# Kernel tuning notes

Measured on AMD Instinct MI355X. Metric: run time of the kernel, lower is better.

## Reference

```python
import jax, jax.numpy as jnp
import numpy as np

B = 16384      # batch of (user, item) interactions
N = 819200     # total packed implicit-history items (~50 per user)
U = 100000     # num_users
I = 100000     # num_items
D = 64         # emb_dim


def setup_inputs() -> dict:
    key = jax.random.key(0)
    ks = jax.random.split(key, 8)
    user_ids = jax.random.randint(ks[0], (B,), 0, U)
    item_ids = jax.random.randint(ks[1], (B,), 0, I)
    offsets = jnp.sort(jax.random.randint(ks[2], (B,), 0, N)).at[0].set(0)
    flat_implicit = jax.random.randint(ks[3], (N,), 0, I)
    user_emb = 0.1 * jax.random.normal(ks[4], (U, D), dtype=jnp.float32)
    item_emb = 0.1 * jax.random.normal(ks[5], (I, D), dtype=jnp.float32)
    implicit_item_emb = 0.1 * jax.random.normal(ks[6], (I, D), dtype=jnp.float32)
    user_bias = jnp.zeros((U, 1), dtype=jnp.float32)
    item_bias = jnp.zeros((I, 1), dtype=jnp.float32)
    global_bias = jnp.zeros((1,), dtype=jnp.float32)
    return {"user_ids": user_ids, "item_ids": item_ids, "offsets": offsets,
            "flat_implicit": flat_implicit, "user_emb": user_emb,
            "item_emb": item_emb, "implicit_item_emb": implicit_item_emb,
            "user_bias": user_bias, "item_bias": item_bias,
            "global_bias": global_bias}


def reference(user_ids, item_ids, offsets, flat_implicit, user_emb, item_emb,
              implicit_item_emb, user_bias, item_bias, global_bias):
    n = flat_implicit.shape[0]
    b = offsets.shape[0]
    u = user_emb[user_ids]                       # [B, D]
    i = item_emb[item_ids]                       # [B, D]
    imp = implicit_item_emb[flat_implicit]       # [N, D]
    # ragged segment ids from start offsets (empty segments get no rows)
    seg_ids = jnp.searchsorted(offsets, jnp.arange(n), side="right") - 1
    summed = jax.ops.segment_sum(imp, seg_ids, num_segments=b)  # [B, D]
    sizes = jnp.diff(jnp.concatenate([offsets, jnp.array([n], dtype=offsets.dtype)]))
    norm = jnp.where(sizes > 0, jnp.sqrt(sizes.astype(jnp.float32)), 1.0)
    final_user = u + summed / norm[:, None]
    dot = jnp.sum(final_user * i, axis=1)        # [B]
    pred = dot + user_bias[user_ids][:, 0] + item_bias[item_ids][:, 0] + global_bias
    return pred
```

## Files before the change

kernel.cpp:

```cpp
#include <hip/hip_runtime.h>
#include <math.h>


#define WAVES_PER_BLOCK 4

#define LOADIDX(d) const int idx##d = __shfl(my_idx, 4*(d) + sub, 64);
#define LOADVAL(d) const float4 v##d = impv[(size_t)idx##d * 16 + l16];
#define ACCUM(d)                                                         \
    if (super + 4*(d) + sub < end) {                                     \
        acc.x += v##d.x; acc.y += v##d.y;                                \
        acc.z += v##d.z; acc.w += v##d.w;                                \
    }

__global__ __launch_bounds__(256, 1) void svdpp_kernel(
    const int* __restrict__ user_ids,
    const int* __restrict__ item_ids,
    const int* __restrict__ offsets,
    const int* __restrict__ flat_implicit,
    const float* __restrict__ user_emb,
    const float* __restrict__ item_emb,
    const float* __restrict__ imp_emb,
    const float* __restrict__ user_bias,
    const float* __restrict__ item_bias,
    const float* __restrict__ global_bias,
    float* __restrict__ out,
    int B, int N)
{
    const int wave = threadIdx.x >> 6;
    const int lane = threadIdx.x & 63;
    const int b = blockIdx.x * WAVES_PER_BLOCK + wave;
    if (b >= B) return;

    const int sub = lane >> 4;
    const int l16 = lane & 15;

    const int start = offsets[b];
    const int end   = (b + 1 < B) ? offsets[b + 1] : N;
    const int n     = end - start;

    const int user = user_ids[b];
    const int item = item_ids[b];

    const float4 i4 = ((const float4*)(item_emb + (size_t)item * 64))[l16];

    const float4* impv = (const float4*)imp_emb;
    float4 acc = make_float4(0.f, 0.f, 0.f, 0.f);

    for (int super = start; super < end; super += 64) {
        const int a = super + lane;
        const int my_idx = flat_implicit[(a < end) ? a : start];

        LOADIDX(0)  LOADIDX(1)  LOADIDX(2)  LOADIDX(3)
        LOADIDX(4)  LOADIDX(5)  LOADIDX(6)  LOADIDX(7)
        LOADIDX(8)  LOADIDX(9)  LOADIDX(10) LOADIDX(11)
        LOADIDX(12) LOADIDX(13) LOADIDX(14) LOADIDX(15)

        LOADVAL(0)  LOADVAL(1)  LOADVAL(2)  LOADVAL(3)
        LOADVAL(4)  LOADVAL(5)  LOADVAL(6)  LOADVAL(7)
        LOADVAL(8)  LOADVAL(9)  LOADVAL(10) LOADVAL(11)
        LOADVAL(12) LOADVAL(13) LOADVAL(14) LOADVAL(15)

        __builtin_amdgcn_sched_barrier(0);

        ACCUM(0)  ACCUM(1)  ACCUM(2)  ACCUM(3)
        ACCUM(4)  ACCUM(5)  ACCUM(6)  ACCUM(7)
        ACCUM(8)  ACCUM(9)  ACCUM(10) ACCUM(11)
        ACCUM(12) ACCUM(13) ACCUM(14) ACCUM(15)
    }

    float ds = acc.x * i4.x + acc.y * i4.y + acc.z * i4.z + acc.w * i4.w;

    const float u_c = user_emb[(size_t)user * 64 + lane];
    const float i_c = item_emb[(size_t)item * 64 + lane];
    float dui = u_c * i_c;

    #pragma unroll
    for (int off = 32; off >= 1; off >>= 1) {
        ds  += __shfl_xor(ds,  off, 64);
        dui += __shfl_xor(dui, off, 64);
    }

    if (lane == 0) {
        const float norm = (n > 0) ? sqrtf((float)n) : 1.0f;
        out[b] = dui + ds / norm + user_bias[user] + item_bias[item]
               + global_bias[0];
    }
}

extern "C" void kernel_launch(void* const* d_in, const int* in_sizes, int n_in,
                              void* d_out, int out_size, void* d_ws, size_t ws_size,
                              hipStream_t stream) {
    const int*   user_ids      = (const int*)  d_in[0];
    const int*   item_ids      = (const int*)  d_in[1];
    const int*   offsets       = (const int*)  d_in[2];
    const int*   flat_implicit = (const int*)  d_in[3];
    const float* user_emb      = (const float*)d_in[4];
    const float* item_emb      = (const float*)d_in[5];
    const float* imp_emb       = (const float*)d_in[6];
    const float* user_bias     = (const float*)d_in[7];
    const float* item_bias     = (const float*)d_in[8];
    const float* global_bias   = (const float*)d_in[9];
    float* out = (float*)d_out;

    const int B = in_sizes[0];
    const int N = in_sizes[3];

    const int grid = (B + WAVES_PER_BLOCK - 1) / WAVES_PER_BLOCK;
    svdpp_kernel<<<grid, WAVES_PER_BLOCK * 64, 0, stream>>>(
        user_ids, item_ids, offsets, flat_implicit,
        user_emb, item_emb, imp_emb,
        user_bias, item_bias, global_bias,
        out, B, N);
}
```

Before: 141.2 us.

## Split into element-parallel gather with atomics and per-row finalize kernel

The single per-row kernel is replaced by three launches. A zero pass clears the output. An element-parallel gather gives each wave 64 consecutive implicit items, finds each item's segment by binary search, dots the partial segment sums with the item embedding and atomically adds them into the output. A finalize kernel then adds the user-item dot, the normalisation and the biases. This targets load imbalance from ragged segment lengths, at the cost of two extra launches, a log(B) binary search per element, and float atomics whose summation order is nondeterministic.

Result: slower. 152.9 us (+8.3%).

```diff
diff --git a/kernel.cpp b/kernel.cpp
--- a/kernel.cpp
+++ b/kernel.cpp
@@ -2,88 +2,131 @@
 #include <math.h>
 
 
-#define WAVES_PER_BLOCK 4
+#define K1_WAVES 4
 
-#define LOADIDX(d) const int idx##d = __shfl(my_idx, 4*(d) + sub, 64);
+__global__ void svdpp_zero(float* __restrict__ out, int B)
+{
+    const int i = blockIdx.x * blockDim.x + threadIdx.x;
+    if (i < B) out[i] = 0.f;
+}
+
+#define LOADIDX(d) const int idx##d = __shfl(my_idx, (sub << 4) | (d), 64);
 #define LOADVAL(d) const float4 v##d = impv[(size_t)idx##d * 16 + l16];
-#define ACCUM(d)                                                         \
-    if (super + 4*(d) + sub < end) {                                     \
-        acc.x += v##d.x; acc.y += v##d.y;                                \
-        acc.z += v##d.z; acc.w += v##d.w;                                \
+
+#define FLUSH()                                                              \
+    {                                                                        \
+        float p = acc.x * i4.x + acc.y * i4.y + acc.z * i4.z + acc.w * i4.w; \
+        p += __shfl_xor(p, 1, 64);                                           \
+        p += __shfl_xor(p, 2, 64);                                           \
+        p += __shfl_xor(p, 4, 64);                                           \
+        p += __shfl_xor(p, 8, 64);                                           \
+        if (l16 == 0) atomicAdd(&out[cur], p);                               \
     }
 
-__global__ __launch_bounds__(256, 1) void svdpp_kernel(
+#define STEP(d)                                                              \
+    {                                                                        \
+        const int sd = __shfl(seg, (sub << 4) | (d), 64);                    \
+        if (sd != cur) {                                                     \
+            FLUSH();                                                         \
+            cur = sd;                                                        \
+            i4  = ((const float4*)(item_emb + (size_t)item_ids[cur] * 64))[l16]; \
+            acc = make_float4(0.f, 0.f, 0.f, 0.f);                           \
+        }                                                                    \
+        if (base + (sub << 4) + (d) < N) {                                   \
+            acc.x += v##d.x; acc.y += v##d.y;                                \
+            acc.z += v##d.z; acc.w += v##d.w;                                \
+        }                                                                    \
+    }
+
+__global__ __launch_bounds__(256, 1) void svdpp_gather(
+    const int* __restrict__ item_ids,
+    const int* __restrict__ offsets,
+    const int* __restrict__ flat_implicit,
+    const float* __restrict__ item_emb,
+    const float* __restrict__ imp_emb,
+    float* __restrict__ out,
+    int B, int N)
+{
+    const int wave = threadIdx.x >> 6;
+    const int lane = threadIdx.x & 63;
+    const int base = (blockIdx.x * K1_WAVES + wave) << 6;
+    if (base >= N) return;
+
+    const int sub = lane >> 4;
+    const int l16 = lane & 15;
+
+    const int a  = base + lane;
+    const int ac = (a < N) ? a : (N - 1);
+
+    const int my_idx = flat_implicit[ac];
+
+    int lo = 0, hi = B;
+    while (lo < hi) {
+        const int mid = (lo + hi) >> 1;
+        if (offsets[mid] <= ac) lo = mid + 1; else hi = mid;
+    }
+    const int seg = lo - 1;
+
+    int cur = __shfl(seg, sub << 4, 64);
+    float4 i4 = ((const float4*)(item_emb + (size_t)item_ids[cur] * 64))[l16];
+    float4 acc = make_float4(0.f, 0.f, 0.f, 0.f);
+
+    const float4* impv = (const float4*)imp_emb;
+    LOADIDX(0)  LOADIDX(1)  LOADIDX(2)  LOADIDX(3)
+    LOADIDX(4)  LOADIDX(5)  LOADIDX(6)  LOADIDX(7)
+    LOADIDX(8)  LOADIDX(9)  LOADIDX(10) LOADIDX(11)
+    LOADIDX(12) LOADIDX(13) LOADIDX(14) LOADIDX(15)
+
+    LOADVAL(0)  LOADVAL(1)  LOADVAL(2)  LOADVAL(3)
+    LOADVAL(4)  LOADVAL(5)  LOADVAL(6)  LOADVAL(7)
+    LOADVAL(8)  LOADVAL(9)  LOADVAL(10) LOADVAL(11)
+    LOADVAL(12) LOADVAL(13) LOADVAL(14) LOADVAL(15)
+
+    __builtin_amdgcn_sched_barrier(0);
+
+    STEP(0)  STEP(1)  STEP(2)  STEP(3)
+    STEP(4)  STEP(5)  STEP(6)  STEP(7)
+    STEP(8)  STEP(9)  STEP(10) STEP(11)
+    STEP(12) STEP(13) STEP(14) STEP(15)
+
+    FLUSH();
+}
+
+__global__ __launch_bounds__(256, 1) void svdpp_final(
     const int* __restrict__ user_ids,
     const int* __restrict__ item_ids,
     const int* __restrict__ offsets,
-    const int* __restrict__ flat_implicit,
     const float* __restrict__ user_emb,
     const float* __restrict__ item_emb,
-    const float* __restrict__ imp_emb,
     const float* __restrict__ user_bias,
     const float* __restrict__ item_bias,
     const float* __restrict__ global_bias,
     float* __restrict__ out,
     int B, int N)
 {
-    const int wave = threadIdx.x >> 6;
-    const int lane = threadIdx.x & 63;
-    const int b = blockIdx.x * WAVES_PER_BLOCK + wave;
+    const int l16 = threadIdx.x & 15;
+    const int b   = blockIdx.x * 16 + (threadIdx.x >> 4);
     if (b >= B) return;
-
-    const int sub = lane >> 4;
-    const int l16 = lane & 15;
-
-    const int start = offsets[b];
-    const int end   = (b + 1 < B) ? offsets[b + 1] : N;
-    const int n     = end - start;
 
     const int user = user_ids[b];
     const int item = item_ids[b];
 
+    const float4 u4 = ((const float4*)(user_emb + (size_t)user * 64))[l16];
     const float4 i4 = ((const float4*)(item_emb + (size_t)item * 64))[l16];
 
-    const float4* impv = (const float4*)imp_emb;
-    float4 acc = make_float4(0.f, 0.f, 0.f, 0.f);
+    float p = u4.x * i4.x + u4.y * i4.y + u4.z * i4.z + u4.w * i4.w;
+    p += __shfl_xor(p, 1, 64);
+    p += __shfl_xor(p, 2, 64);
+    p += __shfl_xor(p, 4, 64);
+    p += __shfl_xor(p, 8, 64);
 
-    for (int super = start; super < end; super += 64) {
-        const int a = super + lane;
-        const int my_idx = flat_implicit[(a < end) ? a : start];
-
-        LOADIDX(0)  LOADIDX(1)  LOADIDX(2)  LOADIDX(3)
-        LOADIDX(4)  LOADIDX(5)  LOADIDX(6)  LOADIDX(7)
-        LOADIDX(8)  LOADIDX(9)  LOADIDX(10) LOADIDX(11)
-        LOADIDX(12) LOADIDX(13) LOADIDX(14) LOADIDX(15)
-
-        LOADVAL(0)  LOADVAL(1)  LOADVAL(2)  LOADVAL(3)
-        LOADVAL(4)  LOADVAL(5)  LOADVAL(6)  LOADVAL(7)
-        LOADVAL(8)  LOADVAL(9)  LOADVAL(10) LOADVAL(11)
-        LOADVAL(12) LOADVAL(13) LOADVAL(14) LOADVAL(15)
-
-        __builtin_amdgcn_sched_barrier(0);
-
-        ACCUM(0)  ACCUM(1)  ACCUM(2)  ACCUM(3)
-        ACCUM(4)  ACCUM(5)  ACCUM(6)  ACCUM(7)
-        ACCUM(8)  ACCUM(9)  ACCUM(10) ACCUM(11)
-        ACCUM(12) ACCUM(13) ACCUM(14) ACCUM(15)
-    }
-
-    float ds = acc.x * i4.x + acc.y * i4.y + acc.z * i4.z + acc.w * i4.w;
-
-    const float u_c = user_emb[(size_t)user * 64 + lane];
-    const float i_c = item_emb[(size_t)item * 64 + lane];
-    float dui = u_c * i_c;
-
-    #pragma unroll
-    for (int off = 32; off >= 1; off >>= 1) {
-        ds  += __shfl_xor(ds,  off, 64);
-        dui += __shfl_xor(dui, off, 64);
-    }
-
-    if (lane == 0) {
-        const float norm = (n > 0) ? sqrtf((float)n) : 1.0f;
-        out[b] = dui + ds / norm + user_bias[user] + item_bias[item]
-               + global_bias[0];
+    if (l16 == 0) {
+        const int start = offsets[b];
+        const int end   = (b + 1 < B) ? offsets[b + 1] : N;
+        const int n     = end - start;
+        const float norm = (n > 0) ? sqrtf((float)n) : 1.f;
+        out[b] = p + out[b] / norm + user_bias[item == item ? user : user]
+               + item_bias[item] + global_bias[0];
     }
 }
 
@@ -105,10 +148,14 @@
     const int B = in_sizes[0];
     const int N = in_sizes[3];
 
-    const int grid = (B + WAVES_PER_BLOCK - 1) / WAVES_PER_BLOCK;
-    svdpp_kernel<<<grid, WAVES_PER_BLOCK * 64, 0, stream>>>(
-        user_ids, item_ids, offsets, flat_implicit,
-        user_emb, item_emb, imp_emb,
-        user_bias, item_bias, global_bias,
-        out, B, N);
+    svdpp_zero<<<(B + 255) / 256, 256, 0, stream>>>(out, B);
+
+    const int waves = (N + 63) / 64;
+    const int g1 = (waves + K1_WAVES - 1) / K1_WAVES;
+    svdpp_gather<<<g1, K1_WAVES * 64, 0, stream>>>(
+        item_ids, offsets, flat_implicit, item_emb, imp_emb, out, B, N);
+
+    svdpp_final<<<(B + 15) / 16, 256, 0, stream>>>(
+        user_ids, item_ids, offsets, user_emb, item_emb,
+        user_bias, item_bias, global_bias, out, B, N);
 }
```

## Partition implicit-row gathers by item index mod 8 across blocks with atomic combine

Applied to the files above, without the earlier changes.

Launches eight times as many blocks. Each block handles only the implicit items whose index mod 8 matches its partition, so each block group touches a smaller slice of the implicit embedding table, which is meant to improve cache locality (for example per-XCD L2). Matching rows are compacted with ballot and ds_permute, partial dot products are combined into a zeroed output with atomicAdd, and the user and bias terms are added once by a designated block. Nontemporal loads are used for the streaming index and item data. The costs are an extra memset, atomics, eight re-reads of the offsets and index lists, and non-deterministic float summation order.

Result: slower. 189.2 us (+34.0%).

```diff
diff --git a/kernel.cpp b/kernel.cpp
--- a/kernel.cpp
+++ b/kernel.cpp
@@ -2,17 +2,16 @@
 #include <math.h>
 
 
-#define WAVES_PER_BLOCK 4
+typedef float f4 __attribute__((ext_vector_type(4)));
 
-#define LOADIDX(d) const int idx##d = __shfl(my_idx, 4*(d) + sub, 64);
-#define LOADVAL(d) const float4 v##d = impv[(size_t)idx##d * 16 + l16];
-#define ACCUM(d)                                                         \
-    if (super + 4*(d) + sub < end) {                                     \
-        acc.x += v##d.x; acc.y += v##d.y;                                \
-        acc.z += v##d.z; acc.w += v##d.w;                                \
-    }
+#define WPB 4
 
-__global__ __launch_bounds__(256, 1) void svdpp_kernel(
+template <typename T>
+__device__ __forceinline__ T ntload(const T* p) {
+    return __builtin_nontemporal_load(const_cast<T*>(p));
+}
+
+__global__ __launch_bounds__(256, 4) void svdpp_gather(
     const int* __restrict__ user_ids,
     const int* __restrict__ item_ids,
     const int* __restrict__ offsets,
@@ -26,64 +25,71 @@
     float* __restrict__ out,
     int B, int N)
 {
+    const int k    = blockIdx.x & 7;
+    const int jb   = blockIdx.x >> 3;
     const int wave = threadIdx.x >> 6;
     const int lane = threadIdx.x & 63;
-    const int b = blockIdx.x * WAVES_PER_BLOCK + wave;
+
+    const int b = jb * WPB + wave;
     if (b >= B) return;
 
     const int sub = lane >> 4;
     const int l16 = lane & 15;
 
-    const int start = offsets[b];
-    const int end   = (b + 1 < B) ? offsets[b + 1] : N;
-    const int n     = end - start;
+    const int s = offsets[b];
+    const int e = (b + 1 < B) ? offsets[b + 1] : N;
+    const int n = e - s;
 
-    const int user = user_ids[b];
     const int item = item_ids[b];
+    const bool designated = (k == (b & 7));
 
-    const float4 i4 = ((const float4*)(item_emb + (size_t)item * 64))[l16];
+    const f4* item4 = (const f4*)item_emb;
+    const f4  i4    = ntload(&item4[(size_t)item * 16 + l16]);
 
-    const float4* impv = (const float4*)imp_emb;
-    float4 acc = make_float4(0.f, 0.f, 0.f, 0.f);
+    const f4* impv = (const f4*)imp_emb;
+    f4 acc = (f4)(0.f);
 
-    for (int super = start; super < end; super += 64) {
-        const int a = super + lane;
-        const int my_idx = flat_implicit[(a < end) ? a : start];
+    for (int base = s; base < e; base += 64) {
+        const int a   = base + lane;
+        const int ac  = (a < e) ? a : s;
+        const int idx = ntload(&flat_implicit[ac]);
 
-        LOADIDX(0)  LOADIDX(1)  LOADIDX(2)  LOADIDX(3)
-        LOADIDX(4)  LOADIDX(5)  LOADIDX(6)  LOADIDX(7)
-        LOADIDX(8)  LOADIDX(9)  LOADIDX(10) LOADIDX(11)
-        LOADIDX(12) LOADIDX(13) LOADIDX(14) LOADIDX(15)
+        const bool q = (a < e) && ((idx & 7) == k);
 
-        LOADVAL(0)  LOADVAL(1)  LOADVAL(2)  LOADVAL(3)
-        LOADVAL(4)  LOADVAL(5)  LOADVAL(6)  LOADVAL(7)
-        LOADVAL(8)  LOADVAL(9)  LOADVAL(10) LOADVAL(11)
-        LOADVAL(12) LOADVAL(13) LOADVAL(14) LOADVAL(15)
+        const unsigned long long m = __ballot(q);
+        const int cnt = __popcll(m);
+        if (cnt == 0) continue;
 
-        __builtin_amdgcn_sched_barrier(0);
+        const int rank = q ? __popcll(m & ((1ull << lane) - 1ull)) : 63;
+        const int cidx = __builtin_amdgcn_ds_permute(rank << 2, idx);
 
-        ACCUM(0)  ACCUM(1)  ACCUM(2)  ACCUM(3)
-        ACCUM(4)  ACCUM(5)  ACCUM(6)  ACCUM(7)
-        ACCUM(8)  ACCUM(9)  ACCUM(10) ACCUM(11)
-        ACCUM(12) ACCUM(13) ACCUM(14) ACCUM(15)
+        for (int t = 0; t < cnt; t += 4) {
+            const int r      = t + sub;
+            const int rowidx = __shfl(cidx, (r < cnt) ? r : 0, 64);
+            const f4  v      = impv[(size_t)(unsigned)rowidx * 16 + l16];
+            if (r < cnt) acc += v;
+        }
     }
 
-    float ds = acc.x * i4.x + acc.y * i4.y + acc.z * i4.z + acc.w * i4.w;
+    const float invn = (n > 0) ? (1.0f / sqrtf((float)n)) : 1.0f;
+    float p = (acc.x * i4.x + acc.y * i4.y + acc.z * i4.z + acc.w * i4.w) * invn;
 
-    const float u_c = user_emb[(size_t)user * 64 + lane];
-    const float i_c = item_emb[(size_t)item * 64 + lane];
-    float dui = u_c * i_c;
+    if (designated && sub == 0) {
+        const f4* user4 = (const f4*)user_emb;
+        const f4 u4 = ntload(&user4[(size_t)user_ids[b] * 16 + l16]);
+        p += u4.x * i4.x + u4.y * i4.y + u4.z * i4.z + u4.w * i4.w;
+    }
 
     #pragma unroll
-    for (int off = 32; off >= 1; off >>= 1) {
-        ds  += __shfl_xor(ds,  off, 64);
-        dui += __shfl_xor(dui, off, 64);
-    }
+    for (int off = 32; off >= 1; off >>= 1)
+        p += __shfl_xor(p, off, 64);
 
     if (lane == 0) {
-        const float norm = (n > 0) ? sqrtf((float)n) : 1.0f;
-        out[b] = dui + ds / norm + user_bias[user] + item_bias[item]
-               + global_bias[0];
+        if (designated)
+            p += ntload(&user_bias[user_ids[b]])
+               + ntload(&item_bias[item])
+               + ntload(&global_bias[0]);
+        atomicAdd(&out[b], p);
     }
 }
 
@@ -105,8 +111,10 @@
     const int B = in_sizes[0];
     const int N = in_sizes[3];
 
-    const int grid = (B + WAVES_PER_BLOCK - 1) / WAVES_PER_BLOCK;
-    svdpp_kernel<<<grid, WAVES_PER_BLOCK * 64, 0, stream>>>(
+    hipMemsetAsync(out, 0, (size_t)B * sizeof(float), stream);
+
+    const int blocks = 8 * ((B + WPB - 1) / WPB);
+    svdpp_gather<<<blocks, WPB * 64, 0, stream>>>(
         user_ids, item_ids, offsets, flat_implicit,
         user_emb, item_emb, imp_emb,
         user_bias, item_bias, global_bias,
```
